# Optimization experiments

Measured on AMD Instinct MI355X. Metric: run time of the kernel, lower is better.

Reference implementation:

```python
import jax, jax.numpy as jnp
import numpy as np

B, S, D = 2, 2048, 1024
H = 16
HD = D // H   # 64
K = 64        # local_window / neighbors per position


def setup_inputs() -> dict:
    key = jax.random.key(0)
    k1, k2, k3, k4, k5, k6 = jax.random.split(key, 6)
    scale = 1.0 / np.sqrt(D)
    x = jax.random.normal(k1, (B, S, D), dtype=jnp.float32)
    routes = jax.random.randint(k2, (S, K), 0, S, dtype=jnp.int64)
    W_qkv = jax.random.normal(k3, (D, 3 * D), dtype=jnp.float32) * scale
    b_qkv = jnp.zeros((3 * D,), dtype=jnp.float32)
    W_proj = jax.random.normal(k4, (D, D), dtype=jnp.float32) * scale
    b_proj = jnp.zeros((D,), dtype=jnp.float32)
    return {"x": x, "W_qkv": W_qkv, "b_qkv": b_qkv,
            "W_proj": W_proj, "b_proj": b_proj, "routes": routes}


def reference(x, W_qkv, b_qkv, W_proj, b_proj, routes):
    # x: (B, S, D)
    qkv = x @ W_qkv + b_qkv                       # (B, S, 3D)
    qkv = qkv.reshape(B, S, 3, H, HD)
    q, k, v = qkv[:, :, 0], qkv[:, :, 1], qkv[:, :, 2]   # (B, S, H, HD)
    q = q.transpose(0, 2, 1, 3)                   # (B, H, S, HD)
    k = k.transpose(0, 2, 1, 3)
    v = v.transpose(0, 2, 1, 3)

    r = jnp.clip(routes, 0, S - 1)                # (S, K)
    # Gather neighbor keys/values: (B, H, S, K, HD)
    k_n = k[:, :, r, :]
    v_n = v[:, :, r, :]

    scores = jnp.einsum('bhsd,bhskd->bhsk', q, k_n) / jnp.sqrt(
        jnp.asarray(HD, dtype=q.dtype))           # (B, H, S, K)
    attn = jax.nn.softmax(scores, axis=-1)
    out = jnp.einsum('bhsk,bhskd->bhsd', attn, v_n)       # (B, H, S, HD)

    out = out.transpose(0, 2, 1, 3).reshape(B, S, D)
    return out @ W_proj + b_proj
```

## Files before the change

### kernel.cpp

```cpp
#include <hip/hip_runtime.h>
#include <stdint.h>

#define B_ 2
#define S_ 2048
#define D_ 1024
#define H_ 16
#define HD_ 64
#define K_ 64

typedef __attribute__((ext_vector_type(8))) __bf16 bf16x8v;
typedef __attribute__((ext_vector_type(4))) float f32x4;
typedef __attribute__((ext_vector_type(8))) unsigned short ushort8v;

#define GLD_LDS16(g, l)                                                        \
  __builtin_amdgcn_global_load_lds(                                            \
      (const __attribute__((address_space(1))) void*)(g),                      \
      (__attribute__((address_space(3))) void*)(l), 16, 0, 0)

__device__ __forceinline__ float bf2f(unsigned short u) {
  union { unsigned u32; float f; } c;
  c.u32 = ((unsigned)u) << 16;
  return c.f;
}
__device__ __forceinline__ unsigned short f2bf(float f) {
  union { float f; unsigned u; } c;
  c.f = f;
  unsigned u = c.u;
  u += 0x7fffu + ((u >> 16) & 1u);
  return (unsigned short)(u >> 16);
}

__global__ __launch_bounds__(256) void prep_fused(
    const float* __restrict__ x, unsigned short* __restrict__ x_bf,
    const float* __restrict__ Wqkv, unsigned short* __restrict__ wqkvT,
    const float* __restrict__ Wproj, unsigned short* __restrict__ wprojT) {
  __shared__ float tile[64][65];
  const int bid = blockIdx.x;
  const int t = threadIdx.x;

  if (bid < 4096) {
    const int i = bid * 256 + t;
    float4 v = ((const float4*)x)[i];
    ushort4 o;
    o.x = f2bf(v.x); o.y = f2bf(v.y); o.z = f2bf(v.z); o.w = f2bf(v.w);
    ((ushort4*)x_bf)[i] = o;
    return;
  }

  const float* W;
  unsigned short* WT;
  int R, C, bx, by;
  if (bid < 4096 + 768) {
    const int b2 = bid - 4096;
    W = Wqkv; WT = wqkvT; R = D_; C = 3 * D_;
    by = b2 / 48; bx = b2 - by * 48;
  } else {
    const int b3 = bid - 4096 - 768;
    W = Wproj; WT = wprojT; R = D_; C = D_;
    by = b3 >> 4; bx = b3 & 15;
  }
  const int r0 = by * 64;
  const int c0 = bx * 64;
#pragma unroll
  for (int i = 0; i < 16; ++i) {
    int idx = t + i * 256;
    int rr = idx >> 6, cc = idx & 63;
    tile[rr][cc] = W[(size_t)(r0 + rr) * C + c0 + cc];
  }
  __syncthreads();
#pragma unroll
  for (int i = 0; i < 16; ++i) {
    int idx = t + i * 256;
    int rr = idx >> 6, cc = idx & 63;
    WT[(size_t)(c0 + rr) * R + r0 + cc] = f2bf(tile[cc][rr]);
  }
}

template <bool OUT_F32>
__global__ __launch_bounds__(256) void gemm_bias(
    const unsigned short* __restrict__ A, const unsigned short* __restrict__ Bt,
    const float* __restrict__ bias, void* __restrict__ Cout,
    int M, int N, int Kd) {
  __shared__ unsigned short As[128 * 64];
  __shared__ unsigned short Bs[128 * 64];
  const int t = threadIdx.x;
  const int w = t >> 6;
  const int l = t & 63;
  const int m0 = blockIdx.y * 128;
  const int n0 = blockIdx.x * 128;
  const int wr = w >> 1, wc = w & 1;

  f32x4 acc[4][4] = {};

  const int g_r = t >> 3;
  const int scol = ((t & 7) * 8) ^ ((g_r & 7) * 8);
  char* asBase = (char*)As + w * 1024;
  char* bsBase = (char*)Bs + w * 1024;

  const int lr = l & 15;
  const int kq = (l >> 4) * 8;
  const int xr = (lr & 7) * 8;

  const int KT = Kd >> 6;
  for (int kt = 0; kt < KT; ++kt) {
    const int k0 = kt << 6;
    {
#pragma unroll
      for (int i = 0; i < 4; ++i)
        GLD_LDS16(A + (size_t)(m0 + i * 32 + g_r) * Kd + k0 + scol,
                  asBase + i * 4096);
#pragma unroll
      for (int i = 0; i < 4; ++i)
        GLD_LDS16(Bt + (size_t)(n0 + i * 32 + g_r) * Kd + k0 + scol,
                  bsBase + i * 4096);
    }
    __syncthreads();
    bf16x8v af[4][2], bfv[4][2];
#pragma unroll
    for (int m = 0; m < 4; ++m) {
      const int row = wr * 64 + m * 16 + lr;
#pragma unroll
      for (int ks = 0; ks < 2; ++ks)
        af[m][ks] = *(const bf16x8v*)&As[row * 64 + ((ks * 32 + kq) ^ xr)];
    }
#pragma unroll
    for (int n = 0; n < 4; ++n) {
      const int row = wc * 64 + n * 16 + lr;
#pragma unroll
      for (int ks = 0; ks < 2; ++ks)
        bfv[n][ks] = *(const bf16x8v*)&Bs[row * 64 + ((ks * 32 + kq) ^ xr)];
    }
#pragma unroll
    for (int m = 0; m < 4; ++m)
#pragma unroll
      for (int n = 0; n < 4; ++n)
#pragma unroll
        for (int ks = 0; ks < 2; ++ks)
          acc[m][n] = __builtin_amdgcn_mfma_f32_16x16x32_bf16(
              af[m][ks], bfv[n][ks], acc[m][n], 0, 0, 0);
    __syncthreads();
  }

  const int rbase = (l >> 4) * 4;
#pragma unroll
  for (int m = 0; m < 4; ++m) {
#pragma unroll
    for (int n = 0; n < 4; ++n) {
      const int gc = n0 + wc * 64 + n * 16 + lr;
      const float bv = bias[gc];
#pragma unroll
      for (int j = 0; j < 4; ++j) {
        const int gr = m0 + wr * 64 + m * 16 + rbase + j;
        float v = acc[m][n][j] + bv;
        if (OUT_F32)
          ((float*)Cout)[(size_t)gr * N + gc] = v;
        else
          ((unsigned short*)Cout)[(size_t)gr * N + gc] = f2bf(v);
      }
    }
  }
}

__global__ __launch_bounds__(256) void attn_kernel(
    const unsigned short* __restrict__ qkv, const int* __restrict__ routes,
    unsigned short* __restrict__ outp) {
  __shared__ float sc[16][68];
  __shared__ unsigned rtsoff[64];
  __shared__ float pbuf[1024];
  const int bs = blockIdx.x;
  const int b = bs >> 11;
  const int s = bs & (S_ - 1);
  const int t = threadIdx.x;
  const int w = t >> 6, l = t & 63;
  const int kh2 = w >> 1, hh = w & 1;

  if (t < 64) {
    int r = routes[s * K_ + t];
    r = min(max(r, 0), S_ - 1);
    rtsoff[t] = (unsigned)(b * S_ + r) * 3072u;
  }
  __syncthreads();

  const unsigned colo = hh * 512 + l * 8;
  const int head = colo >> 6;
  const size_t rowbase = (size_t)bs * 3072;

  float q[8];
  {
    ushort8v u = *(const ushort8v*)(qkv + rowbase + colo);
#pragma unroll
    for (int i = 0; i < 8; ++i) q[i] = bf2f(u[i]) * 0.125f;
  }

  const unsigned kofs = 1024u + colo;
  const unsigned vofs = 2048u + colo;
  const int jbase = kh2 * 32;

#pragma unroll 4
  for (int j2 = 0; j2 < 32; ++j2) {
    const int j = jbase + j2;
    ushort8v u = *(const ushort8v*)(qkv + (rtsoff[j] + kofs));
    float d = q[0] * bf2f(u[0]);
#pragma unroll
    for (int i = 1; i < 8; ++i) d += q[i] * bf2f(u[i]);
    d += __shfl_xor(d, 1);
    d += __shfl_xor(d, 2);
    d += __shfl_xor(d, 4);
    if ((l & 7) == 0) sc[head][j] = d;
  }
  __syncthreads();

  {
    const int h = t >> 4;
    const int l2 = t & 15;
    float v0 = sc[h][l2], v1 = sc[h][l2 + 16], v2 = sc[h][l2 + 32],
          v3 = sc[h][l2 + 48];
    float m = fmaxf(fmaxf(v0, v1), fmaxf(v2, v3));
    m = fmaxf(m, __shfl_xor(m, 1));
    m = fmaxf(m, __shfl_xor(m, 2));
    m = fmaxf(m, __shfl_xor(m, 4));
    m = fmaxf(m, __shfl_xor(m, 8));
    v0 = __expf(v0 - m); v1 = __expf(v1 - m);
    v2 = __expf(v2 - m); v3 = __expf(v3 - m);
    float ss = v0 + v1 + v2 + v3;
    ss += __shfl_xor(ss, 1);
    ss += __shfl_xor(ss, 2);
    ss += __shfl_xor(ss, 4);
    ss += __shfl_xor(ss, 8);
    float inv = 1.0f / ss;
    sc[h][l2] = v0 * inv;
    sc[h][l2 + 16] = v1 * inv;
    sc[h][l2 + 32] = v2 * inv;
    sc[h][l2 + 48] = v3 * inv;
  }
  __syncthreads();

  float acc[8] = {};
#pragma unroll 4
  for (int j2 = 0; j2 < 32; ++j2) {
    const int j = jbase + j2;
    ushort8v u = *(const ushort8v*)(qkv + (rtsoff[j] + vofs));
    const float p = sc[head][j];
#pragma unroll
    for (int i = 0; i < 8; ++i) acc[i] += p * bf2f(u[i]);
  }

  if (kh2 == 1) {
    f32x4 a0 = {acc[0], acc[1], acc[2], acc[3]};
    f32x4 a1 = {acc[4], acc[5], acc[6], acc[7]};
    *(f32x4*)&pbuf[colo] = a0;
    *(f32x4*)&pbuf[colo + 4] = a1;
  }
  __syncthreads();
  if (kh2 == 0) {
    ushort8v o;
#pragma unroll
    for (int i = 0; i < 8; ++i) o[i] = f2bf(acc[i] + pbuf[colo + i]);
    *(ushort8v*)(outp + (size_t)bs * D_ + colo) = o;
  }
}

extern "C" void kernel_launch(void* const* d_in, const int* in_sizes, int n_in,
                              void* d_out, int out_size, void* d_ws,
                              size_t ws_size, hipStream_t stream) {
  const float* x = (const float*)d_in[0];
  const float* Wqkv = (const float*)d_in[1];
  const float* bqkv = (const float*)d_in[2];
  const float* Wproj = (const float*)d_in[3];
  const float* bproj = (const float*)d_in[4];
  const int* routes = (const int*)d_in[5];
  float* out = (float*)d_out;

  char* ws = (char*)d_ws;
  unsigned short* x_bf = (unsigned short*)(ws);
  unsigned short* wqkvT = (unsigned short*)(ws + 8388608);
  unsigned short* wprojT = (unsigned short*)(ws + 14680064);
  unsigned short* qkv = (unsigned short*)(ws + 16777216);
  unsigned short* aout = (unsigned short*)(ws + 41943040);

  prep_fused<<<5120, 256, 0, stream>>>(x, x_bf, Wqkv, wqkvT, Wproj, wprojT);

  gemm_bias<false><<<dim3(3 * D_ / 128, B_ * S_ / 128), 256, 0, stream>>>(
      x_bf, wqkvT, bqkv, qkv, B_ * S_, 3 * D_, D_);
  attn_kernel<<<B_ * S_, 256, 0, stream>>>(qkv, routes, aout);
  gemm_bias<true><<<dim3(D_ / 128, B_ * S_ / 128), 256, 0, stream>>>(
      aout, wprojT, bproj, out, B_ * S_, D_, D_);
}
```

Baseline: 136.0 us.

## Double-buffer LDS tiles in GEMM to overlap global loads with MFMA

```diff
diff --git a/kernel.cpp b/kernel.cpp
--- a/kernel.cpp
+++ b/kernel.cpp
@@ -81,8 +81,8 @@
     const unsigned short* __restrict__ A, const unsigned short* __restrict__ Bt,
     const float* __restrict__ bias, void* __restrict__ Cout,
     int M, int N, int Kd) {
-  __shared__ unsigned short As[128 * 64];
-  __shared__ unsigned short Bs[128 * 64];
+  __shared__ unsigned short As[2][128 * 64];
+  __shared__ unsigned short Bs[2][128 * 64];
   const int t = threadIdx.x;
   const int w = t >> 6;
   const int l = t & 63;
@@ -101,34 +101,40 @@
   const int kq = (l >> 4) * 8;
   const int xr = (lr & 7) * 8;
 
+#define STAGE_AB(kt, buf)                                                      \
+  {                                                                            \
+    _Pragma("unroll") for (int i = 0; i < 4; ++i)                              \
+        GLD_LDS16(A + (size_t)(m0 + i * 32 + g_r) * Kd + (kt) * 64 + scol,     \
+                  asBase + (buf) * 16384 + i * 4096);                          \
+    _Pragma("unroll") for (int i = 0; i < 4; ++i)                              \
+        GLD_LDS16(Bt + (size_t)(n0 + i * 32 + g_r) * Kd + (kt) * 64 + scol,    \
+                  bsBase + (buf) * 16384 + i * 4096);                          \
+  }
+
   const int KT = Kd >> 6;
+  STAGE_AB(0, 0);
+  __syncthreads();
+
+  int cur = 0;
   for (int kt = 0; kt < KT; ++kt) {
-    const int k0 = kt << 6;
-    {
-#pragma unroll
-      for (int i = 0; i < 4; ++i)
-        GLD_LDS16(A + (size_t)(m0 + i * 32 + g_r) * Kd + k0 + scol,
-                  asBase + i * 4096);
-#pragma unroll
-      for (int i = 0; i < 4; ++i)
-        GLD_LDS16(Bt + (size_t)(n0 + i * 32 + g_r) * Kd + k0 + scol,
-                  bsBase + i * 4096);
-    }
-    __syncthreads();
+    if (kt + 1 < KT) STAGE_AB(kt + 1, cur ^ 1);
+
     bf16x8v af[4][2], bfv[4][2];
 #pragma unroll
     for (int m = 0; m < 4; ++m) {
       const int row = wr * 64 + m * 16 + lr;
 #pragma unroll
       for (int ks = 0; ks < 2; ++ks)
-        af[m][ks] = *(const bf16x8v*)&As[row * 64 + ((ks * 32 + kq) ^ xr)];
+        af[m][ks] =
+            *(const bf16x8v*)&As[cur][row * 64 + ((ks * 32 + kq) ^ xr)];
     }
 #pragma unroll
     for (int n = 0; n < 4; ++n) {
       const int row = wc * 64 + n * 16 + lr;
 #pragma unroll
       for (int ks = 0; ks < 2; ++ks)
-        bfv[n][ks] = *(const bf16x8v*)&Bs[row * 64 + ((ks * 32 + kq) ^ xr)];
+        bfv[n][ks] =
+            *(const bf16x8v*)&Bs[cur][row * 64 + ((ks * 32 + kq) ^ xr)];
     }
 #pragma unroll
     for (int m = 0; m < 4; ++m)
@@ -138,8 +144,11 @@
         for (int ks = 0; ks < 2; ++ks)
           acc[m][n] = __builtin_amdgcn_mfma_f32_16x16x32_bf16(
               af[m][ks], bfv[n][ks], acc[m][n], 0, 0, 0);
+
     __syncthreads();
-  }
+    cur ^= 1;
+  }
+#undef STAGE_AB
 
   const int rbase = (l >> 4) * 4;
 #pragma unroll
```

Result: slower. 139.0 us (+2.2%).
